# Kernel tuning notes

Hardware: AMD Instinct MI355X
Metric: run time of the kernel (lower is better)

Reference implementation:

```python
import jax, jax.numpy as jnp
import numpy as np

N_NODES = 50000
NEG_SLOPE = 0.2  # DGL GATConv default


def _leaky_relu(x):
    return jnp.where(x >= 0, x, NEG_SLOPE * x)


def gat_conv(h, W, al, ar, src, dst, activate):
    # h: [N, F_in], W: [F_in, H, D], al/ar: [H, D]
    fs = jnp.einsum('nf,fhd->nhd', h, W)          # [N, H, D]
    el = jnp.sum(fs * al, axis=-1)                 # [N, H]
    er = jnp.sum(fs * ar, axis=-1)                 # [N, H]
    e = _leaky_relu(el[src] + er[dst])             # [E, H]
    # numerically stable edge softmax per destination node
    m = jax.ops.segment_max(e, dst, num_segments=N_NODES)   # [N, H]
    ex = jnp.exp(e - m[dst])                                  # [E, H]
    s = jax.ops.segment_sum(ex, dst, num_segments=N_NODES)  # [N, H]
    alpha = ex / s[dst]                                       # [E, H]
    msg = alpha[:, :, None] * fs[src]                          # [E, H, D]
    out = jax.ops.segment_sum(msg, dst, num_segments=N_NODES) # [N, H, D]
    if activate:
        out = jax.nn.relu(out)
    return out


def setup_inputs() -> dict:
    key = jax.random.key(0)
    ks = jax.random.split(key, 12)
    E = 1600000
    H, D, Fin, C = 4, 32, 100, 47
    inp = {
        'x': jax.random.normal(ks[0], (N_NODES, Fin), jnp.float32),
        'W0': jax.random.normal(ks[1], (Fin, H, D), jnp.float32) * 0.1,
        'al0': jax.random.normal(ks[2], (H, D), jnp.float32) * 0.1,
        'ar0': jax.random.normal(ks[3], (H, D), jnp.float32) * 0.1,
        'W1': jax.random.normal(ks[4], (H * D, H, D), jnp.float32) * 0.1,
        'al1': jax.random.normal(ks[5], (H, D), jnp.float32) * 0.1,
        'ar1': jax.random.normal(ks[6], (H, D), jnp.float32) * 0.1,
        'W2': jax.random.normal(ks[7], (H * D, H, C), jnp.float32) * 0.1,
        'al2': jax.random.normal(ks[8], (H, C), jnp.float32) * 0.1,
        'ar2': jax.random.normal(ks[9], (H, C), jnp.float32) * 0.1,
        'src': jax.random.randint(ks[10], (E,), 0, N_NODES, jnp.int32),
        'dst': jax.random.randint(ks[11], (E,), 0, N_NODES, jnp.int32),
    }
    return inp


def reference(x, W0, al0, ar0, W1, al1, ar1, W2, al2, ar2, src, dst):
    h = gat_conv(x, W0, al0, ar0, src, dst, True)            # [N, H, D]
    h = h.reshape(h.shape[0], -1)                             # flatten(1)
    h = gat_conv(h, W1, al1, ar1, src, dst, True)
    h = h.reshape(h.shape[0], -1)
    h = gat_conv(h, W2, al2, ar2, src, dst, False)           # [N, H, C]
    h = h.mean(axis=1)                                        # mean over heads
    return jax.nn.log_softmax(h, axis=-1)                     # [N, C]
```

## Files before the change

### kernel.cpp

```cpp
#include <hip/hip_runtime.h>
#include <hip/hip_bf16.h>


using bf16 = __hip_bfloat16;
typedef __attribute__((ext_vector_type(8))) short short8;
typedef __attribute__((ext_vector_type(4))) float floatx4;

static constexpr int NN = 50000;
static constexpr int H  = 4;

__device__ __forceinline__ float b2f(bf16 x) { return __bfloat162float(x); }
__device__ __forceinline__ float ldx(const void* p, size_t i, bool bf) {
    return bf ? __bfloat162float(((const bf16*)p)[i]) : ((const float*)p)[i];
}
__device__ __forceinline__ unsigned short f2b_bits(float v) {
    bf16 h = __float2bfloat16(v);
    return *reinterpret_cast<unsigned short*>(&h);
}
__device__ __forceinline__ unsigned short w_bits(const void* p, size_t i, bool bf) {
    if (bf) return ((const unsigned short*)p)[i];
    return f2b_bits(((const float*)p)[i]);
}
__device__ __forceinline__ float bl(unsigned u) { return __uint_as_float(u << 16); }
__device__ __forceinline__ float bh(unsigned u) { return __uint_as_float(u & 0xFFFF0000u); }

__global__ void detect_k(const void* __restrict__ x, int* __restrict__ flag) {
    __shared__ int cnt;
    if (threadIdx.x == 0) cnt = 0;
    __syncthreads();
    const unsigned short* u = (const unsigned short*)x;
    unsigned short b = u[threadIdx.x * 2];
    int e = (b >> 7) & 0xFF;
    if (e >= 0x70 && e <= 0x8F) atomicAdd(&cnt, 1);
    __syncthreads();
    if (threadIdx.x == 0) *flag = (cnt > 128) ? 1 : 0;
}

__global__ void xpad_k(const void* __restrict__ x, bf16* __restrict__ xp,
                       const int* __restrict__ flag, int total) {
    int i = blockIdx.x * 256 + threadIdx.x;
    if (i >= total) return;
    const bool bf = (*flag != 0);
    int n = i >> 7, k = i & 127;
    float v = (k < 100) ? ldx(x, (size_t)n * 100 + k, bf) : 0.f;
    xp[i] = __float2bfloat16(v);
}

__global__ void deg_k(const int* __restrict__ dst, int* __restrict__ deg,
                      unsigned short* __restrict__ slot16, int E) {
    int e = blockIdx.x * 256 + threadIdx.x;
    if (e >= E) return;
    int p = atomicAdd(&deg[dst[e]], 1);
    slot16[e] = (unsigned short)p;
}

__global__ void scan1_k(const int* __restrict__ deg, int* __restrict__ rowptr,
                        int* __restrict__ bsum, int N) {
    __shared__ int buf[256];
    int tid = threadIdx.x, i = blockIdx.x * 256 + tid;
    int v = (i < N) ? deg[i] : 0;
    buf[tid] = v;
    __syncthreads();
    for (int off = 1; off < 256; off <<= 1) {
        int t = (tid >= off) ? buf[tid - off] : 0;
        __syncthreads();
        buf[tid] += t;
        __syncthreads();
    }
    if (i < N) rowptr[i] = buf[tid] - v;
    if (tid == 255) bsum[blockIdx.x] = buf[255];
}

__global__ void scan2_k(const int* __restrict__ bsum, int* __restrict__ boff, int nb) {
    __shared__ int buf[256];
    int tid = threadIdx.x;
    int v = (tid < nb) ? bsum[tid] : 0;
    buf[tid] = v;
    __syncthreads();
    for (int off = 1; off < 256; off <<= 1) {
        int t = (tid >= off) ? buf[tid - off] : 0;
        __syncthreads();
        buf[tid] += t;
        __syncthreads();
    }
    if (tid < nb) boff[tid] = buf[tid] - v;
}

__global__ void scan3_k(int* __restrict__ rowptr, const int* __restrict__ boff,
                        int N, int E) {
    int i = blockIdx.x * 256 + threadIdx.x;
    if (i < N) rowptr[i] += boff[blockIdx.x];
    if (i == 0) rowptr[N] = E;
}

__global__ void fill_k(const int* __restrict__ src, const int* __restrict__ dst,
                       const int* __restrict__ rowptr,
                       const unsigned short* __restrict__ slot16,
                       unsigned short* __restrict__ col16, int E) {
    int e = blockIdx.x * 256 + threadIdx.x;
    if (e >= E) return;
    int d = dst[e];
    col16[rowptr[d] + slot16[e]] = (unsigned short)src[e];
}

template <int KW, int M, int S, int HS, int HW>
__global__ void __launch_bounds__(256) gemm_k(const bf16* __restrict__ in,
                                              const void* __restrict__ W,
                                              const void* __restrict__ al,
                                              const void* __restrict__ ar,
                                              bf16* __restrict__ fs,
                                              float* __restrict__ el,
                                              float* __restrict__ er,
                                              const int* __restrict__ flag, int N) {
    constexpr int CT  = S / 16;
    constexpr int WST = 136;
    __shared__ short wlds[S * WST];
    const bool bf = (*flag != 0);
    const int tid = threadIdx.x;

    for (int idx = tid; idx < 64 * S; idx += 256) {
        int k2 = idx / S, p = idx % S;
        int j = p % HS, h = p / HS;
        int c = h * HW + j;
        bool valid = (j < HW);
        int k0 = 2 * k2;
        unsigned short u0 = (valid && k0 < KW)     ? w_bits(W, (size_t)k0 * M + c, bf)       : 0;
        unsigned short u1 = (valid && k0 + 1 < KW) ? w_bits(W, (size_t)(k0 + 1) * M + c, bf) : 0;
        *(unsigned*)&wlds[p * WST + 2 * k2] = (unsigned)u0 | ((unsigned)u1 << 16);
    }
    __syncthreads();

    const int wave = tid >> 6, lane = tid & 63;
    const int q = lane >> 4, l16 = lane & 15;
    const int base = blockIdx.x * 128;

    floatx4 acc[2][CT] = {};

#pragma unroll
    for (int chunk = 0; chunk < 4; ++chunk) {
        const int kb = chunk * 32 + q * 8;
        short8 a0 = {}, a1 = {};
        const int n0 = base + wave * 16 + l16;
        const int n1 = n0 + 64;
        if (n0 < N) a0 = *(const short8*)(in + (size_t)n0 * 128 + kb);
        if (n1 < N) a1 = *(const short8*)(in + (size_t)n1 * 128 + kb);
#pragma unroll
        for (int ct = 0; ct < CT; ++ct) {
            const int p = ct * 16 + l16;
            short8 b = *(const short8*)&wlds[p * WST + kb];
            acc[0][ct] = __builtin_amdgcn_mfma_f32_16x16x32_bf16(a0, b, acc[0][ct], 0, 0, 0);
            acc[1][ct] = __builtin_amdgcn_mfma_f32_16x16x32_bf16(a1, b, acc[1][ct], 0, 0, 0);
        }
    }

#pragma unroll
    for (int rt = 0; rt < 2; ++rt) {
        const int tb = base + rt * 64 + wave * 16;
#pragma unroll
        for (int ct = 0; ct < CT; ++ct) {
            const int p = ct * 16 + l16;
#pragma unroll
            for (int r = 0; r < 4; ++r) {
                int node = tb + q * 4 + r;
                if (node < N) fs[(size_t)node * S + p] = __float2bfloat16(acc[rt][ct][r]);
            }
        }
    }

    float* red = (float*)wlds;
#pragma unroll
    for (int rt = 0; rt < 2; ++rt) {
        __syncthreads();
        float elp[4][4] = {}, erp[4][4] = {};
#pragma unroll
        for (int ct = 0; ct < CT; ++ct) {
            const int p = ct * 16 + l16;
            const int j = p % HS, h = p / HS;
            const bool valid = (j < HW);
            float alc = valid ? ldx(al, h * HW + j, bf) : 0.f;
            float arc = valid ? ldx(ar, h * HW + j, bf) : 0.f;
#pragma unroll
            for (int r = 0; r < 4; ++r) {
                float v = acc[rt][ct][r];
#pragma unroll
                for (int h2 = 0; h2 < 4; ++h2) {
                    elp[r][h2] += (h == h2) ? v * alc : 0.f;
                    erp[r][h2] += (h == h2) ? v * arc : 0.f;
                }
            }
        }
#pragma unroll
        for (int r = 0; r < 4; ++r)
#pragma unroll
            for (int h2 = 0; h2 < 4; ++h2) {
                int slot = (wave * 128) + (q * 32) + (r * 8) + (h2 * 2);
                red[slot * 16 + l16] = elp[r][h2];
                red[(slot + 1) * 16 + l16] = erp[r][h2];
            }
        __syncthreads();
#pragma unroll
        for (int pass = 0; pass < 2; ++pass) {
            int slot = tid + pass * 256;
            float sum = 0.f;
#pragma unroll
            for (int j = 0; j < 16; ++j) sum += red[slot * 16 + j];
            int which = slot & 1;
            int h2 = (slot >> 1) & 3;
            int r  = (slot >> 3) & 3;
            int qq = (slot >> 5) & 3;
            int wv = slot >> 7;
            int node = base + rt * 64 + wv * 16 + qq * 4 + r;
            if (node < N) {
                if (which == 0) el[(size_t)node * 4 + h2] = sum;
                else            er[(size_t)node * 4 + h2] = sum;
            }
        }
    }
}

template <bool RELU>
__global__ void __launch_bounds__(256) agg01_k(const float* __restrict__ el,
                                               const float* __restrict__ er,
                                               const bf16* __restrict__ fs,
                                               const int* __restrict__ rowptr,
                                               const unsigned short* __restrict__ col,
                                               bf16* __restrict__ out, int N) {
    const int wave = threadIdx.x >> 6, lane = threadIdx.x & 63;
    const int d = blockIdx.x * 4 + wave;
    __shared__ float wrow[4][16][4];
    __shared__ int   scol[4][16];
    if (d >= N) return;
    const int rs = rowptr[d], re = rowptr[d + 1];
    const int g = lane >> 4, lg = lane & 15;
    const int c0 = lg * 8;

    if (re == rs) {
        if (g == 0) *(uint4*)(out + (size_t)d * 128 + c0) = make_uint4(0, 0, 0, 0);
        return;
    }

    float4 er4 = *(const float4*)(er + (size_t)d * 4);
    float er_d[4] = {er4.x, er4.y, er4.z, er4.w};

    const int eh = lane >> 2;
    const int hh = lane & 3;
    const int h0 = lg >> 2;

    float acc[8] = {0, 0, 0, 0, 0, 0, 0, 0};
    float swp = 0.f;

    for (int cs = rs; cs < re; cs += 16) {
        int ne = min(16, re - cs);
        if (eh < ne) {
            int s = (int)col[cs + eh];
            if (hh == 0) scol[wave][eh] = s;
            float x = el[(size_t)s * 4 + hh] + er_d[hh];
            x = x >= 0.f ? x : 0.2f * x;
            float w = __expf(x);
            wrow[wave][eh][hh] = w;
            swp += w;
        }
#pragma unroll 4
        for (int e = g; e < ne; e += 4) {
            int s = scol[wave][e];
            float w = wrow[wave][e][h0];
            uint4 u = *(const uint4*)(fs + (size_t)s * 128 + c0);
            acc[0] += w * bl(u.x); acc[1] += w * bh(u.x);
            acc[2] += w * bl(u.y); acc[3] += w * bh(u.y);
            acc[4] += w * bl(u.z); acc[5] += w * bh(u.z);
            acc[6] += w * bl(u.w); acc[7] += w * bh(u.w);
        }
    }

#pragma unroll
    for (int k = 0; k < 8; ++k) {
        acc[k] += __shfl_xor(acc[k], 16);
        acc[k] += __shfl_xor(acc[k], 32);
    }
#pragma unroll
    for (int off = 4; off < 64; off <<= 1) swp += __shfl_xor(swp, off);
    float sh = __shfl(swp, h0);

    if (g == 0) {
        float inv = 1.0f / sh;
        float v[8];
#pragma unroll
        for (int k = 0; k < 8; ++k) {
            v[k] = acc[k] * inv;
            if (RELU) v[k] = fmaxf(v[k], 0.f);
        }
        uint4 o;
        o.x = (unsigned)f2b_bits(v[0]) | ((unsigned)f2b_bits(v[1]) << 16);
        o.y = (unsigned)f2b_bits(v[2]) | ((unsigned)f2b_bits(v[3]) << 16);
        o.z = (unsigned)f2b_bits(v[4]) | ((unsigned)f2b_bits(v[5]) << 16);
        o.w = (unsigned)f2b_bits(v[6]) | ((unsigned)f2b_bits(v[7]) << 16);
        *(uint4*)(out + (size_t)d * 128 + c0) = o;
    }
}

__global__ void __launch_bounds__(192) agg2_k(const float* __restrict__ el,
                                              const float* __restrict__ er,
                                              const bf16* __restrict__ fs,
                                              const int* __restrict__ rowptr,
                                              const unsigned short* __restrict__ col,
                                              void* __restrict__ out,
                                              const int* __restrict__ flag) {
    constexpr int HS = 48, S = 192, LPG = 24, TPB = 192;
    constexpr int NG = TPB / LPG;
    constexpr int CH = TPB / 4;
    constexpr int NW = TPB / 64;
    const int d = blockIdx.x;
    const int tid = threadIdx.x;
    const bool bf = (*flag != 0);
    const int rs = rowptr[d], re = rowptr[d + 1];

    __shared__ float wrow[CH][4];
    __shared__ int scol_s[CH];
    __shared__ float part[NG][S];
    __shared__ float red2[NW][4];
    __shared__ float sh_s[4];
    __shared__ float vout[S];

    if (re == rs) {
        if (tid < 47) {
            float r = -logf(47.f);
            if (bf) ((bf16*)out)[(size_t)d * 47 + tid] = __float2bfloat16(r);
            else    ((float*)out)[(size_t)d * 47 + tid] = r;
        }
        return;
    }

    float4 er4 = *(const float4*)(er + (size_t)d * 4);
    float er_d[4] = {er4.x, er4.y, er4.z, er4.w};

    const int g  = tid / LPG;
    const int lg = tid % LPG;
    const int c0 = lg * 8;
    const int h0 = c0 / HS;

    float acc[8] = {0, 0, 0, 0, 0, 0, 0, 0};
    float swpart = 0.f;

    for (int cs = rs; cs < re; cs += CH) {
        int ne = min(CH, re - cs);
        if (tid < ne * 4) {
            int j = tid >> 2, h = tid & 3;
            int s = (int)col[cs + j];
            if (h == 0) scol_s[j] = s;
            float x = el[(size_t)s * 4 + h] + er_d[h];
            x = x >= 0.f ? x : 0.2f * x;
            float w = __expf(x);
            wrow[j][h] = w;
            swpart += w;
        }
        __syncthreads();
#pragma unroll 4
        for (int e = g; e < ne; e += NG) {
            int s = scol_s[e];
            uint4 u = *(const uint4*)(fs + (size_t)s * S + c0);
            float w = wrow[e][h0];
            acc[0] += w * bl(u.x); acc[1] += w * bh(u.x);
            acc[2] += w * bl(u.y); acc[3] += w * bh(u.y);
            acc[4] += w * bl(u.z); acc[5] += w * bh(u.z);
            acc[6] += w * bl(u.w); acc[7] += w * bh(u.w);
        }
        __syncthreads();
    }

    float sw = swpart;
#pragma unroll
    for (int off = 4; off < 64; off <<= 1) sw += __shfl_xor(sw, off);
    const int wave = tid >> 6, lane = tid & 63;
    if (lane < 4) red2[wave][lane] = sw;
#pragma unroll
    for (int k = 0; k < 8; ++k) part[g][c0 + k] = acc[k];
    __syncthreads();
    if (tid < 4) {
        float s = 0.f;
#pragma unroll
        for (int w = 0; w < NW; ++w) s += red2[w][tid];
        sh_s[tid] = s;
    }
    __syncthreads();

    if (tid < S / 4) {
        int c = tid * 4;
        float4 v = make_float4(0, 0, 0, 0);
#pragma unroll
        for (int gg = 0; gg < NG; ++gg) {
            v.x += part[gg][c + 0]; v.y += part[gg][c + 1];
            v.z += part[gg][c + 2]; v.w += part[gg][c + 3];
        }
        float is = 1.0f / sh_s[c / HS];
        vout[c + 0] = v.x * is; vout[c + 1] = v.y * is;
        vout[c + 2] = v.z * is; vout[c + 3] = v.w * is;
    }
    __syncthreads();

    if (tid < 64) {
        int c = tid;
        float val = 0.f, vm = -INFINITY;
        if (c < 47) {
            val = 0.25f * (vout[c] + vout[48 + c] + vout[96 + c] + vout[144 + c]);
            vm = val;
        }
        float m = vm;
#pragma unroll
        for (int off = 32; off >= 1; off >>= 1) m = fmaxf(m, __shfl_xor(m, off));
        float ex = (c < 47) ? __expf(val - m) : 0.f;
        float s = ex;
#pragma unroll
        for (int off = 32; off >= 1; off >>= 1) s += __shfl_xor(s, off);
        if (c < 47) {
            float r = val - m - logf(s);
            if (bf) ((bf16*)out)[(size_t)d * 47 + c] = __float2bfloat16(r);
            else    ((float*)out)[(size_t)d * 47 + c] = r;
        }
    }
}

extern "C" void kernel_launch(void* const* d_in, const int* in_sizes, int n_in,
                              void* d_out, int out_size, void* d_ws, size_t ws_size,
                              hipStream_t stream) {
    const void* x   = d_in[0];
    const void* W0  = d_in[1];
    const void* al0 = d_in[2];
    const void* ar0 = d_in[3];
    const void* W1  = d_in[4];
    const void* al1 = d_in[5];
    const void* ar1 = d_in[6];
    const void* W2  = d_in[7];
    const void* al2 = d_in[8];
    const void* ar2 = d_in[9];
    const int* src  = (const int*)d_in[10];
    const int* dst  = (const int*)d_in[11];
    const int E = in_sizes[10];
    const int N = NN;

    bf16* fs    = (bf16*)d_ws;
    bf16* hb16  = fs + (size_t)N * 192;
    bf16* xpad  = hb16 + (size_t)N * 128;
    float* el   = (float*)(xpad + (size_t)N * 128);
    float* er   = el + (size_t)N * H;
    int* rowptr = (int*)(er + (size_t)N * H);
    int* deg    = rowptr + (N + 1);
    unsigned short* col16  = (unsigned short*)(deg + N);
    unsigned short* slot16 = col16 + E;
    int* bsum   = (int*)(slot16 + E);
    int* boff   = bsum + 256;
    int* flag   = boff + 256;

    const int gN  = (N + 255) / 256;
    const int gE  = (E + 255) / 256;
    const int gG  = (N + 127) / 128;
    const int gA  = (N + 3) / 4;

    detect_k<<<1, 256, 0, stream>>>(x, flag);
    xpad_k<<<(N * 128 + 255) / 256, 256, 0, stream>>>(x, xpad, flag, N * 128);

    hipMemsetAsync(deg, 0, (size_t)N * 4, stream);
    deg_k<<<gE, 256, 0, stream>>>(dst, deg, slot16, E);
    scan1_k<<<gN, 256, 0, stream>>>(deg, rowptr, bsum, N);
    scan2_k<<<1, 256, 0, stream>>>(bsum, boff, gN);
    scan3_k<<<gN, 256, 0, stream>>>(rowptr, boff, N, E);
    fill_k<<<gE, 256, 0, stream>>>(src, dst, rowptr, slot16, col16, E);

    gemm_k<100, 128, 128, 32, 32><<<gG, 256, 0, stream>>>(
        xpad, W0, al0, ar0, fs, el, er, flag, N);
    agg01_k<true><<<gA, 256, 0, stream>>>(el, er, fs, rowptr, col16, hb16, N);

    gemm_k<128, 128, 128, 32, 32><<<gG, 256, 0, stream>>>(
        hb16, W1, al1, ar1, fs, el, er, flag, N);
    agg01_k<true><<<gA, 256, 0, stream>>>(el, er, fs, rowptr, col16, hb16, N);

    gemm_k<128, 188, 192, 48, 47><<<gG, 256, 0, stream>>>(
        hb16, W2, al2, ar2, fs, el, er, flag, N);
    agg2_k<<<N, 192, 0, stream>>>(el, er, fs, rowptr, col16, d_out, flag);
}
```

Before: 534.3 us.

## Store features head-major and aggregate one head per block pass

The change stores projected features, attention logits and aggregated outputs in head-major layout ([H][N][D]). Each aggregation block now handles a single head, so the per-head gathered feature table is a quarter the size and may fit better in cache. Aggregation kernels take 64 edges per wave iteration, and the last layer's log-softmax moves into a separate final kernel reading a new per-head out2 buffer. In exchange, every edge's column and logit reads are repeated four times, and the change adds an extra kernel launch plus a round trip through memory.

```diff
diff --git a/kernel.cpp b/kernel.cpp
--- a/kernel.cpp
+++ b/kernel.cpp
@@ -103,7 +103,7 @@
     col16[rowptr[d] + slot16[e]] = (unsigned short)src[e];
 }
 
-template <int KW, int M, int S, int HS, int HW>
+template <int KW, int M, int S, int HS, int HW, bool IN_HM>
 __global__ void __launch_bounds__(256) gemm_k(const bf16* __restrict__ in,
                                               const void* __restrict__ W,
                                               const void* __restrict__ al,
@@ -142,8 +142,14 @@
         short8 a0 = {}, a1 = {};
         const int n0 = base + wave * 16 + l16;
         const int n1 = n0 + 64;
-        if (n0 < N) a0 = *(const short8*)(in + (size_t)n0 * 128 + kb);
-        if (n1 < N) a1 = *(const short8*)(in + (size_t)n1 * 128 + kb);
+        if (IN_HM) {
+            const bf16* sl = in + (size_t)chunk * N * 32 + q * 8;
+            if (n0 < N) a0 = *(const short8*)(sl + (size_t)n0 * 32);
+            if (n1 < N) a1 = *(const short8*)(sl + (size_t)n1 * 32);
+        } else {
+            if (n0 < N) a0 = *(const short8*)(in + (size_t)n0 * 128 + kb);
+            if (n1 < N) a1 = *(const short8*)(in + (size_t)n1 * 128 + kb);
+        }
 #pragma unroll
         for (int ct = 0; ct < CT; ++ct) {
             const int p = ct * 16 + l16;
@@ -159,10 +165,12 @@
 #pragma unroll
         for (int ct = 0; ct < CT; ++ct) {
             const int p = ct * 16 + l16;
+            const int h = p / HS, j = p % HS;
+            bf16* dstp = fs + ((size_t)h * N) * HS + j;
 #pragma unroll
             for (int r = 0; r < 4; ++r) {
                 int node = tb + q * 4 + r;
-                if (node < N) fs[(size_t)node * S + p] = __float2bfloat16(acc[rt][ct][r]);
+                if (node < N) dstp[(size_t)node * HS] = __float2bfloat16(acc[rt][ct][r]);
             }
         }
     }
@@ -211,78 +219,84 @@
             int wv = slot >> 7;
             int node = base + rt * 64 + wv * 16 + qq * 4 + r;
             if (node < N) {
-                if (which == 0) el[(size_t)node * 4 + h2] = sum;
-                else            er[(size_t)node * 4 + h2] = sum;
+                if (which == 0) el[(size_t)h2 * N + node] = sum;
+                else            er[(size_t)h2 * N + node] = sum;
             }
         }
     }
 }
 
 template <bool RELU>
-__global__ void __launch_bounds__(256) agg01_k(const float* __restrict__ el,
-                                               const float* __restrict__ er,
-                                               const bf16* __restrict__ fs,
-                                               const int* __restrict__ rowptr,
-                                               const unsigned short* __restrict__ col,
-                                               bf16* __restrict__ out, int N) {
+__global__ void __launch_bounds__(256) agg01h_k(const float* __restrict__ el,
+                                                const float* __restrict__ er,
+                                                const bf16* __restrict__ fs,
+                                                const int* __restrict__ rowptr,
+                                                const unsigned short* __restrict__ col,
+                                                bf16* __restrict__ out, int N) {
+    const int per = (N + 3) / 4;
+    const int h = blockIdx.x / per;
+    const int blk = blockIdx.x - h * per;
     const int wave = threadIdx.x >> 6, lane = threadIdx.x & 63;
-    const int d = blockIdx.x * 4 + wave;
-    __shared__ float wrow[4][16][4];
-    __shared__ int   scol[4][16];
+    const int d = blk * 4 + wave;
+    __shared__ float wlds[4][64];
+    __shared__ int   scol[4][64];
     if (d >= N) return;
     const int rs = rowptr[d], re = rowptr[d + 1];
-    const int g = lane >> 4, lg = lane & 15;
+    const int lg = lane & 3;
     const int c0 = lg * 8;
+    bf16* orow = out + ((size_t)h * N + d) * 32 + c0;
 
     if (re == rs) {
-        if (g == 0) *(uint4*)(out + (size_t)d * 128 + c0) = make_uint4(0, 0, 0, 0);
+        if (lane < 4) *(uint4*)orow = make_uint4(0, 0, 0, 0);
         return;
     }
 
-    float4 er4 = *(const float4*)(er + (size_t)d * 4);
-    float er_d[4] = {er4.x, er4.y, er4.z, er4.w};
-
-    const int eh = lane >> 2;
-    const int hh = lane & 3;
-    const int h0 = lg >> 2;
-
+    const float er_d = er[(size_t)h * N + d];
+    const bf16* fsl = fs + (size_t)h * N * 32;
+    const float* ell = el + (size_t)h * N;
+
+    const int eb = lane >> 2;
     float acc[8] = {0, 0, 0, 0, 0, 0, 0, 0};
     float swp = 0.f;
 
-    for (int cs = rs; cs < re; cs += 16) {
-        int ne = min(16, re - cs);
-        if (eh < ne) {
-            int s = (int)col[cs + eh];
-            if (hh == 0) scol[wave][eh] = s;
-            float x = el[(size_t)s * 4 + hh] + er_d[hh];
+    for (int cs = rs; cs < re; cs += 64) {
+        int ne = min(64, re - cs);
+        if (lane < ne) {
+            int s = (int)col[cs + lane];
+            scol[wave][lane] = s;
+            float x = ell[s] + er_d;
             x = x >= 0.f ? x : 0.2f * x;
             float w = __expf(x);
-            wrow[wave][eh][hh] = w;
+            wlds[wave][lane] = w;
             swp += w;
         }
-#pragma unroll 4
-        for (int e = g; e < ne; e += 4) {
-            int s = scol[wave][e];
-            float w = wrow[wave][e][h0];
-            uint4 u = *(const uint4*)(fs + (size_t)s * 128 + c0);
-            acc[0] += w * bl(u.x); acc[1] += w * bh(u.x);
-            acc[2] += w * bl(u.y); acc[3] += w * bh(u.y);
-            acc[4] += w * bl(u.z); acc[5] += w * bh(u.z);
-            acc[6] += w * bl(u.w); acc[7] += w * bh(u.w);
+#pragma unroll
+        for (int k = 0; k < 4; ++k) {
+            int e = eb + k * 16;
+            if (e < ne) {
+                int s = scol[wave][e];
+                float w = wlds[wave][e];
+                uint4 u = *(const uint4*)(fsl + (size_t)s * 32 + c0);
+                acc[0] += w * bl(u.x); acc[1] += w * bh(u.x);
+                acc[2] += w * bl(u.y); acc[3] += w * bh(u.y);
+                acc[4] += w * bl(u.z); acc[5] += w * bh(u.z);
+                acc[6] += w * bl(u.w); acc[7] += w * bh(u.w);
+            }
         }
     }
 
 #pragma unroll
     for (int k = 0; k < 8; ++k) {
+        acc[k] += __shfl_xor(acc[k], 4);
+        acc[k] += __shfl_xor(acc[k], 8);
         acc[k] += __shfl_xor(acc[k], 16);
         acc[k] += __shfl_xor(acc[k], 32);
     }
 #pragma unroll
-    for (int off = 4; off < 64; off <<= 1) swp += __shfl_xor(swp, off);
-    float sh = __shfl(swp, h0);
-
-    if (g == 0) {
-        float inv = 1.0f / sh;
+    for (int off = 1; off < 64; off <<= 1) swp += __shfl_xor(swp, off);
+
+    if (lane < 4) {
+        float inv = 1.0f / swp;
         float v[8];
 #pragma unroll
         for (int k = 0; k < 8; ++k) {
@@ -294,128 +308,110 @@
         o.y = (unsigned)f2b_bits(v[2]) | ((unsigned)f2b_bits(v[3]) << 16);
         o.z = (unsigned)f2b_bits(v[4]) | ((unsigned)f2b_bits(v[5]) << 16);
         o.w = (unsigned)f2b_bits(v[6]) | ((unsigned)f2b_bits(v[7]) << 16);
-        *(uint4*)(out + (size_t)d * 128 + c0) = o;
-    }
-}
-
-__global__ void __launch_bounds__(192) agg2_k(const float* __restrict__ el,
-                                              const float* __restrict__ er,
-                                              const bf16* __restrict__ fs,
-                                              const int* __restrict__ rowptr,
-                                              const unsigned short* __restrict__ col,
-                                              void* __restrict__ out,
-                                              const int* __restrict__ flag) {
-    constexpr int HS = 48, S = 192, LPG = 24, TPB = 192;
-    constexpr int NG = TPB / LPG;
-    constexpr int CH = TPB / 4;
-    constexpr int NW = TPB / 64;
-    const int d = blockIdx.x;
-    const int tid = threadIdx.x;
-    const bool bf = (*flag != 0);
+        *(uint4*)orow = o;
+    }
+}
+
+__global__ void __launch_bounds__(256) agg2h_k(const float* __restrict__ el,
+                                               const float* __restrict__ er,
+                                               const bf16* __restrict__ fs,
+                                               const int* __restrict__ rowptr,
+                                               const unsigned short* __restrict__ col,
+                                               bf16* __restrict__ out2, int N) {
+    const int per = (N + 3) / 4;
+    const int h = blockIdx.x / per;
+    const int blk = blockIdx.x - h * per;
+    const int wave = threadIdx.x >> 6, lane = threadIdx.x & 63;
+    const int d = blk * 4 + wave;
+    __shared__ float wlds[4][64];
+    __shared__ int   scol[4][64];
+    __shared__ float part[4][10][48];
+    if (d >= N) return;
     const int rs = rowptr[d], re = rowptr[d + 1];
-
-    __shared__ float wrow[CH][4];
-    __shared__ int scol_s[CH];
-    __shared__ float part[NG][S];
-    __shared__ float red2[NW][4];
-    __shared__ float sh_s[4];
-    __shared__ float vout[S];
+    bf16* orow = out2 + ((size_t)h * N + d) * 48;
 
     if (re == rs) {
-        if (tid < 47) {
-            float r = -logf(47.f);
-            if (bf) ((bf16*)out)[(size_t)d * 47 + tid] = __float2bfloat16(r);
-            else    ((float*)out)[(size_t)d * 47 + tid] = r;
-        }
+        if (lane < 48) orow[lane] = __float2bfloat16(0.f);
         return;
     }
 
-    float4 er4 = *(const float4*)(er + (size_t)d * 4);
-    float er_d[4] = {er4.x, er4.y, er4.z, er4.w};
-
-    const int g  = tid / LPG;
-    const int lg = tid % LPG;
+    const float er_d = er[(size_t)h * N + d];
+    const bf16* fsl = fs + (size_t)h * N * 48;
+    const float* ell = el + (size_t)h * N;
+
+    const int l6 = lane / 6;
+    const int lg = lane - l6 * 6;
     const int c0 = lg * 8;
-    const int h0 = c0 / HS;
+    const bool act = (lane < 60);
 
     float acc[8] = {0, 0, 0, 0, 0, 0, 0, 0};
-    float swpart = 0.f;
-
-    for (int cs = rs; cs < re; cs += CH) {
-        int ne = min(CH, re - cs);
-        if (tid < ne * 4) {
-            int j = tid >> 2, h = tid & 3;
-            int s = (int)col[cs + j];
-            if (h == 0) scol_s[j] = s;
-            float x = el[(size_t)s * 4 + h] + er_d[h];
+    float swp = 0.f;
+
+    for (int cs = rs; cs < re; cs += 64) {
+        int ne = min(64, re - cs);
+        if (lane < ne) {
+            int s = (int)col[cs + lane];
+            scol[wave][lane] = s;
+            float x = ell[s] + er_d;
             x = x >= 0.f ? x : 0.2f * x;
             float w = __expf(x);
-            wrow[j][h] = w;
-            swpart += w;
-        }
-        __syncthreads();
-#pragma unroll 4
-        for (int e = g; e < ne; e += NG) {
-            int s = scol_s[e];
-            uint4 u = *(const uint4*)(fs + (size_t)s * S + c0);
-            float w = wrow[e][h0];
-            acc[0] += w * bl(u.x); acc[1] += w * bh(u.x);
-            acc[2] += w * bl(u.y); acc[3] += w * bh(u.y);
-            acc[4] += w * bl(u.z); acc[5] += w * bh(u.z);
-            acc[6] += w * bl(u.w); acc[7] += w * bh(u.w);
-        }
-        __syncthreads();
-    }
-
-    float sw = swpart;
-#pragma unroll
-    for (int off = 4; off < 64; off <<= 1) sw += __shfl_xor(sw, off);
-    const int wave = tid >> 6, lane = tid & 63;
-    if (lane < 4) red2[wave][lane] = sw;
-#pragma unroll
-    for (int k = 0; k < 8; ++k) part[g][c0 + k] = acc[k];
-    __syncthreads();
-    if (tid < 4) {
-        float s = 0.f;
-#pragma unroll
-        for (int w = 0; w < NW; ++w) s += red2[w][tid];
-        sh_s[tid] = s;
-    }
-    __syncthreads();
-
-    if (tid < S / 4) {
-        int c = tid * 4;
-        float4 v = make_float4(0, 0, 0, 0);
-#pragma unroll
-        for (int gg = 0; gg < NG; ++gg) {
-            v.x += part[gg][c + 0]; v.y += part[gg][c + 1];
-            v.z += part[gg][c + 2]; v.w += part[gg][c + 3];
-        }
-        float is = 1.0f / sh_s[c / HS];
-        vout[c + 0] = v.x * is; vout[c + 1] = v.y * is;
-        vout[c + 2] = v.z * is; vout[c + 3] = v.w * is;
-    }
-    __syncthreads();
-
-    if (tid < 64) {
-        int c = tid;
-        float val = 0.f, vm = -INFINITY;
-        if (c < 47) {
-            val = 0.25f * (vout[c] + vout[48 + c] + vout[96 + c] + vout[144 + c]);
-            vm = val;
-        }
-        float m = vm;
-#pragma unroll
-        for (int off = 32; off >= 1; off >>= 1) m = fmaxf(m, __shfl_xor(m, off));
-        float ex = (c < 47) ? __expf(val - m) : 0.f;
-        float s = ex;
-#pragma unroll
-        for (int off = 32; off >= 1; off >>= 1) s += __shfl_xor(s, off);
-        if (c < 47) {
-            float r = val - m - logf(s);
-            if (bf) ((bf16*)out)[(size_t)d * 47 + c] = __float2bfloat16(r);
-            else    ((float*)out)[(size_t)d * 47 + c] = r;
-        }
+            wlds[wave][lane] = w;
+            swp += w;
+        }
+#pragma unroll
+        for (int k = 0; k < 7; ++k) {
+            int e = l6 + k * 10;
+            if (act && e < ne) {
+                int s = scol[wave][e];
+                float w = wlds[wave][e];
+                uint4 u = *(const uint4*)(fsl + (size_t)s * 48 + c0);
+                acc[0] += w * bl(u.x); acc[1] += w * bh(u.x);
+                acc[2] += w * bl(u.y); acc[3] += w * bh(u.y);
+                acc[4] += w * bl(u.z); acc[5] += w * bh(u.z);
+                acc[6] += w * bl(u.w); acc[7] += w * bh(u.w);
+            }
+        }
+    }
+
+    if (act) {
+        *(float4*)&part[wave][l6][c0]     = make_float4(acc[0], acc[1], acc[2], acc[3]);
+        *(float4*)&part[wave][l6][c0 + 4] = make_float4(acc[4], acc[5], acc[6], acc[7]);
+    }
+#pragma unroll
+    for (int off = 1; off < 64; off <<= 1) swp += __shfl_xor(swp, off);
+
+    if (lane < 48) {
+        float v = 0.f;
+#pragma unroll
+        for (int i = 0; i < 10; ++i) v += part[wave][i][lane];
+        orow[lane] = __float2bfloat16(v / swp);
+    }
+}
+
+__global__ void final_k(const bf16* __restrict__ out2, void* __restrict__ out,
+                        const int* __restrict__ flag, int N) {
+    int n = blockIdx.x;
+    int c = threadIdx.x;
+    const bool bf = (*flag != 0);
+    float val = 0.f, vm = -INFINITY;
+    if (c < 47) {
+        val = 0.25f * (b2f(out2[((size_t)0 * N + n) * 48 + c]) +
+                       b2f(out2[((size_t)1 * N + n) * 48 + c]) +
+                       b2f(out2[((size_t)2 * N + n) * 48 + c]) +
+                       b2f(out2[((size_t)3 * N + n) * 48 + c]));
+        vm = val;
+    }
+    float m = vm;
+#pragma unroll
+    for (int off = 32; off >= 1; off >>= 1) m = fmaxf(m, __shfl_xor(m, off));
+    float ex = (c < 47) ? __expf(val - m) : 0.f;
+    float s = ex;
+#pragma unroll
+    for (int off = 32; off >= 1; off >>= 1) s += __shfl_xor(s, off);
+    if (c < 47) {
+        float r = val - m - logf(s);
+        if (bf) ((bf16*)out)[(size_t)n * 47 + c] = __float2bfloat16(r);
+        else    ((float*)out)[(size_t)n * 47 + c] = r;
     }
 }
 
@@ -440,7 +436,8 @@
     bf16* fs    = (bf16*)d_ws;
     bf16* hb16  = fs + (size_t)N * 192;
     bf16* xpad  = hb16 + (size_t)N * 128;
-    float* el   = (float*)(xpad + (size_t)N * 128);
+    bf16* out2  = xpad + (size_t)N * 128;
+    float* el   = (float*)(out2 + (size_t)N * 192);
     float* er   = el + (size_t)N * H;
     int* rowptr = (int*)(er + (size_t)N * H);
     int* deg    = rowptr + (N + 1);
@@ -453,7 +450,7 @@
     const int gN  = (N + 255) / 256;
     const int gE  = (E + 255) / 256;
     const int gG  = (N + 127) / 128;
-    const int gA  = (N + 3) / 4;
+    const int gA  = 4 * ((N + 3) / 4);
 
     detect_k<<<1, 256, 0, stream>>>(x, flag);
     xpad_k<<<(N * 128 + 255) / 256, 256, 0, stream>>>(x, xpad, flag, N * 128);
@@ -465,15 +462,17 @@
     scan3_k<<<gN, 256, 0, stream>>>(rowptr, boff, N, E);
     fill_k<<<gE, 256, 0, stream>>>(src, dst, rowptr, slot16, col16, E);
 
-    gemm_k<100, 128, 128, 32, 32><<<gG, 256, 0, stream>>>(
+    gemm_k<100, 128, 128, 32, 32, false><<<gG, 256, 0, stream>>>(
         xpad, W0, al0, ar0, fs, el, er, flag, N);
-    agg01_k<true><<<gA, 256, 0, stream>>>(el, er, fs, rowptr, col16, hb16, N);
-
-    gemm_k<128, 128, 128, 32, 32><<<gG, 256, 0, stream>>>(
+    agg01h_k<true><<<gA, 256, 0, stream>>>(el, er, fs, rowptr, col16, hb16, N);
+
+    gemm_k<128, 128, 128, 32, 32, true><<<gG, 256, 0, stream>>>(
         hb16, W1, al1, ar1, fs, el, er, flag, N);
-    agg01_k<true><<<gA, 256, 0, stream>>>(el, er, fs, rowptr, col16, hb16, N);
-
-    gemm_k<128, 188, 192, 48, 47><<<gG, 256, 0, stream>>>(
+    agg01h_k<true><<<gA, 256, 0, stream>>>(el, er, fs, rowptr, col16, hb16, N);
+
+    gemm_k<128, 188, 192, 48, 47, true><<<gG, 256, 0, stream>>>(
         hb16, W2, al2, ar2, fs, el, er, flag, N);
-    agg2_k<<<N, 192, 0, stream>>>(el, er, fs, rowptr, col16, d_out, flag);
-}
+    agg2h_k<<<gA, 256, 0, stream>>>(el, er, fs, rowptr, col16, out2, N);
+
+    final_k<<<N, 64, 0, stream>>>(out2, d_out, flag, N);
+}
```

Result: slower. 644.3 us (+20.6%).
